# Performance work log

Hardware: AMD Instinct MI355X
Metric: run time of the kernel (lower is better)

Reference implementation:

```python
import jax, jax.numpy as jnp
import numpy as np

# Module hyperparameters (BNMorph.__init__ defaults + KITTI resolution)
B, H, W = 8, 320, 1024
SEARCH_W = 7      # serachWidth
SEARCH_H = 3      # searchHeight
SPARSITY_RAD = 2
SENSE_R = 20
PIX_DW = 24.0     # pixel_distance_weight
ALPHA_DW = 0.7    # alpha_distance_weight
PIX_MUL_DW = 1.9  # pixel_mulline_distance_weight
ALPHA_PAD = 1.6   # alpha_padding
EDGE_DENSITY = 0.02


def _make_offsets():
    # Exactly mirrors BNMorph.__init__ buffer construction.
    rs = np.arange(-SEARCH_W, SEARCH_W + 1)
    cs = np.arange(-SEARCH_H, SEARCH_H + 1)
    xx, yy = np.meshgrid(rs, cs)
    xx = xx.flatten(); yy = yy.flatten()
    idx = np.argsort(xx ** 2 + yy ** 2)
    xx = xx[idx]; yy = yy[idx]
    ss = np.arange(-SPARSITY_RAD, SPARSITY_RAD + 1)
    sxx, syy = np.meshgrid(ss, ss)
    sxx = sxx.flatten(); syy = syy.flatten()
    cspan = np.arange(-SENSE_R, SENSE_R + 1)
    cxx, cyy = np.meshgrid(cspan, cspan)
    cxx = cxx.flatten(); cyy = cyy.flatten()
    ci = np.argsort(cxx ** 2 + cyy ** 2)
    cxx = cxx[ci]; cyy = cyy[ci]
    f32 = lambda a: jnp.asarray(a, dtype=jnp.float32)
    return f32(xx), f32(yy), f32(sxx), f32(syy), f32(cxx), f32(cyy)


def setup_inputs() -> dict:
    key = jax.random.key(0)
    k1, k2 = jax.random.split(key)
    binMapsrc = (jax.random.uniform(k1, (B, 1, H, W)) < EDGE_DENSITY).astype(jnp.float32)
    binMapdst = (jax.random.uniform(k2, (B, 1, H, W)) < EDGE_DENSITY).astype(jnp.float32)
    xx, yy, sxx, syy, cxx, cyy = _make_offsets()
    return {"binMapsrc": binMapsrc, "binMapdst": binMapdst,
            "xx": xx, "yy": yy, "sxx": sxx, "syy": syy, "cxx": cxx, "cyy": cyy}


def _forward(binMapsrc, binMapdst, xx, yy, sxx, syy, cxx, cyy):
    src = binMapsrc[:, 0] > 0.5  # [B,H,W] bool
    dst = binMapdst[:, 0] > 0.5
    b, h, w = src.shape

    # ---- 1. sparsity filtering of src edge points ----
    # keep an active pixel iff no active pixel precedes it (raster order)
    # inside the sparsity window -> approximates greedy sparsification.
    sdx = sxx.astype(jnp.int32); sdy = syy.astype(jnp.int32)
    prec = ((sdy < 0) | ((sdy == 0) & (sdx < 0))).astype(jnp.float32)
    Ps = jnp.pad(src.astype(jnp.float32),
                 ((0, 0), (SPARSITY_RAD, SPARSITY_RAD), (SPARSITY_RAD, SPARSITY_RAD)))

    def sp_step(acc, off):
        dx, dy, wk = off
        sl = jax.lax.dynamic_slice(Ps, (0, SPARSITY_RAD + dy, SPARSITY_RAD + dx), (b, h, w))
        return acc + sl * wk, None

    acc, _ = jax.lax.scan(sp_step, jnp.zeros((b, h, w), jnp.float32), (sdx, sdy, prec))
    kept = src & (acc < 0.5)

    # ---- 2. windowed nearest-correspondence search in dst ----
    # offsets (xx,yy) are pre-sorted by distance, so the first hit is nearest.
    qdx = xx.astype(jnp.int32); qdy = yy.astype(jnp.int32)
    Pd = jnp.pad(dst, ((0, 0), (SEARCH_H, SEARCH_H), (SEARCH_W, SEARCH_W)))

    def m_step(carry, off):
        found, vx, vy = carry
        dx, dy, dxf, dyf = off
        sl = jax.lax.dynamic_slice(Pd, (0, SEARCH_H + dy, SEARCH_W + dx), (b, h, w))
        hit = sl & kept & (~found)
        vx = jnp.where(hit, dxf, vx)
        vy = jnp.where(hit, dyf, vy)
        return (found | hit, vx, vy), None

    init = (jnp.zeros((b, h, w), bool),
            jnp.zeros((b, h, w), jnp.float32),
            jnp.zeros((b, h, w), jnp.float32))
    (found, vx, vy), _ = jax.lax.scan(m_step, init, (qdx, qdy, xx, yy))

    # ---- 3. distance-weighted morph field (splat = depthwise conv) ----
    d = jnp.sqrt(cxx ** 2 + cyy ** 2)
    wts = ALPHA_DW * jnp.exp(-d * PIX_MUL_DW / PIX_DW)
    R = SENSE_R
    K = jnp.zeros((2 * R + 1, 2 * R + 1), jnp.float32)
    K = K.at[cyy.astype(jnp.int32) + R, cxx.astype(jnp.int32) + R].set(wts)

    m = found.astype(jnp.float32)
    inp = jnp.stack([m, m * vx, m * vy], axis=1)        # [B,3,H,W]
    ker = jnp.tile(K[None, None], (3, 1, 1, 1))          # [3,1,41,41]
    out = jax.lax.conv_general_dilated(
        inp, ker, (1, 1), ((R, R), (R, R)),
        dimension_numbers=("NCHW", "OIHW", "NCHW"), feature_group_count=3)
    den = out[:, 0] + ALPHA_PAD
    dispx = out[:, 1] / den
    dispy = out[:, 2] / den

    ygrid, xgrid = jnp.meshgrid(jnp.arange(h, dtype=jnp.float32),
                                jnp.arange(w, dtype=jnp.float32), indexing="ij")
    morphedx = xgrid + dispx
    morphedy = ygrid + dispy
    orgpts_x = xgrid * m
    orgpts_y = ygrid * m
    correspts_x = (xgrid + vx) * m
    correspts_y = (ygrid + vy) * m
    return morphedx, morphedy, orgpts_x, orgpts_y, correspts_x, correspts_y


def reference(binMapsrc, binMapdst, xx, yy, sxx, syy, cxx, cyy):
    return _forward(binMapsrc, binMapdst, xx, yy, sxx, syy, cxx, cyy)
```

## Files before the change

kernel.cpp:

```cpp
#include <hip/hip_runtime.h>


#define BB 8
#define HH 320
#define WW 1024
#define N_PIX (BB*HH*WW)
#define WPI (HH*(WW/32))
#define RR 20
#define TLW 64
#define TLH 32
#define TXN (WW/TLW)
#define TYN (HH/TLH)
#define NQ 105
#define CAP 192
#define WSTRIDE 52
#define WTABN (2*42*WSTRIDE)
#define WTAB_OFF (2*BB*WPI*4)

typedef unsigned long long u64;
typedef float v2f __attribute__((ext_vector_type(2)));

__global__ __launch_bounds__(256) void pack_zero(
    const float* __restrict__ src, const float* __restrict__ dst,
    unsigned* __restrict__ packed, float* __restrict__ wtab_g)
{
    int t = threadIdx.x;
    int i = blockIdx.x * 256 + t;
    if (i < WTABN) {
        int rot = i / (42 * WSTRIDE);
        int rem = i - rot * (42 * WSTRIDE);
        int row = rem / WSTRIDE, c = rem - row * WSTRIDE;
        int pc = c + rot;
        float v = 0.0f;
        if (row <= 40 && pc >= 4 && pc <= 44) {
            int dxv = pc - 24, dyv = row - 20;
            float d = sqrtf((float)(dxv * dxv + dyv * dyv));
            v = 0.7f * expf((-d * 1.9f) / 24.0f);
        }
        wtab_g[i] = v;
    }
    const float4* p = (i < (N_PIX >> 2)) ? (const float4*)src + i
                                         : (const float4*)dst + (i - (N_PIX >> 2));
    float4 v = *p;
    unsigned nib = (v.x > 0.5f ? 1u : 0u) | (v.y > 0.5f ? 2u : 0u)
                 | (v.z > 0.5f ? 4u : 0u) | (v.w > 0.5f ? 8u : 0u);
    unsigned val = nib << ((t & 7) * 4);
    val |= __shfl_xor(val, 1);
    val |= __shfl_xor(val, 2);
    val |= __shfl_xor(val, 4);
    if ((t & 7) == 0) packed[i >> 3] = val;
}

__global__ __launch_bounds__(256, 5) void fused_morph(
    const unsigned* __restrict__ packed,
    const float* __restrict__ xx, const float* __restrict__ yy,
    const float* __restrict__ wtab_g,
    float* __restrict__ out)
{
    __shared__ __align__(16) float wtab[WTABN];
    __shared__ unsigned sSrc[74][6];
    __shared__ unsigned sDst[78][6];
    __shared__ __align__(16) unsigned sPt[CAP];
    __shared__ __align__(16) unsigned sWav[4][200];
    __shared__ int prank[NQ];
    __shared__ unsigned char sVB[TLH * TLW];
    __shared__ int lcnt;

    int t = threadIdx.x;
    int txT = blockIdx.x, tyT = blockIdx.y, b = blockIdx.z;
    int tx0 = txT * TLW, ty0 = tyT * TLH;
    int wb0 = (tx0 >> 5) - 1;
    const unsigned* psrc = packed + (size_t)b * WPI;
    const unsigned* pdst = packed + (size_t)(BB + b) * WPI;

    for (int i = t; i < WTABN / 4; i += 256)
        ((float4*)wtab)[i] = ((const float4*)wtab_g)[i];
    for (int i = t; i < 74 * 4; i += 256) {
        int r = i >> 2, w = (i & 3) + 1;
        int gy = ty0 - 22 + r, gw = wb0 + (w - 1);
        sSrc[r][w] = (gy >= 0 && gy < HH && gw >= 0 && gw < 32) ? psrc[(gy << 5) + gw] : 0u;
    }
    for (int i = t; i < 78 * 4; i += 256) {
        int r = i >> 2, w = (i & 3) + 1;
        int gy = ty0 - 23 + r, gw = wb0 + (w - 1);
        sDst[r][w] = (gy >= 0 && gy < HH && gw >= 0 && gw < 32) ? pdst[(gy << 5) + gw] : 0u;
    }
    if (t < 78) { sDst[t][0] = 0; sDst[t][5] = 0; if (t < 74) { sSrc[t][0] = 0; sSrc[t][5] = 0; } }
    if (t < NQ) {
        int dx = (int)xx[t], dy = (int)yy[t];
        prank[(dy + 3) * 15 + (dx + 7)] = (t << 8) | ((dx + 7) << 4) | (dy + 3);
    }
    ((unsigned*)sVB)[t] = 0; ((unsigned*)sVB)[t + 256] = 0;
    if (t == 0) lcnt = 0;
    __syncthreads();

    for (int task = t; task < 288; task += 256) {
        int cr = task >> 2, w = (task & 3) + 1;
        unsigned C = sSrc[cr + 2][w];
        unsigned found = 0;
        if (C) {
            #define EXT5(row) ( (u64)((row)[w-1] >> 30) \
                              | ((u64)(row)[w] << 2) \
                              | ((u64)((row)[w+1] & 3u) << 34) )
            u64 a = EXT5(sSrc[cr]) | EXT5(sSrc[cr + 1]);
            u64 or5 = a | (a >> 1) | (a >> 2) | (a >> 3) | (a >> 4);
            u64 e2 = EXT5(sSrc[cr + 2]);
            unsigned kept = C & ~(unsigned)(or5 | e2 | (e2 >> 1));
            if (kept) {
                u64 dil = 0;
                #pragma unroll
                for (int rr = 0; rr < 7; ++rr) {
                    const unsigned* row = sDst[cr + rr];
                    dil |= (u64)(row[w-1] >> 25) | ((u64)row[w] << 7)
                         | ((u64)(row[w+1] & 0x7Fu) << 39);
                }
                u64 a2 = dil | (dil >> 1);
                u64 b2 = a2 | (a2 >> 2);
                u64 c2 = b2 | (b2 >> 4);
                u64 o15 = c2 | (c2 >> 7);
                found = kept & (unsigned)o15;
            }
        }
        if (w == 1) found &= 0xFFFFF000u;
        if (w == 4) found &= 0x000FFFFFu;
        if (found) {
            int nf = __popc(found);
            int base = atomicAdd(&lcnt, nf);
            unsigned fi = found;
            while (fi) {
                int bit = __builtin_ctz(fi); fi &= fi - 1;
                int px = tx0 - 32 + ((w - 1) << 5) + bit;
                if (base < CAP) sPt[base] = (unsigned)((cr << 10) | px);
                ++base;
            }
        }
    }
    __syncthreads();
    int nPts = lcnt; if (nPts > CAP) nPts = CAP;

    if (t < nPts) {
        unsigned e = sPt[t];
        int cr = (int)(e >> 10), px = (int)(e & 1023u);
        int q = px - tx0 + 25;
        int widx = 1 + (q >> 5), sh = q & 31;
        u64 lo = 0, hi = 0;
        #pragma unroll
        for (int rr = 0; rr < 7; ++rr) {
            const unsigned* row = sDst[cr + rr];
            u64 win = (((u64)row[widx] | ((u64)row[widx + 1] << 32)) >> sh) & 0x7FFFull;
            if (rr < 4) lo |= win << (15 * rr);
            else        hi |= win << (15 * (rr - 4));
        }
        int minv = 0x7FFFFFFF;
        while (lo) { int bb2 = __builtin_ctzll(lo); lo &= lo - 1; int rv = prank[bb2];      if (rv < minv) minv = rv; }
        while (hi) { int bb2 = __builtin_ctzll(hi); hi &= hi - 1; int rv = prank[60 + bb2]; if (rv < minv) minv = rv; }
        int vxp7 = (minv >> 4) & 15, vyp3 = minv & 15;
        int py = ty0 - 20 + cr;
        sPt[t] = (unsigned)px | ((unsigned)py << 10)
               | ((unsigned)vxp7 << 19) | ((unsigned)vyp3 << 23);
        if (px >= tx0 && px < tx0 + TLW && cr >= 20 && cr < 20 + TLH)
            sVB[(cr - 20) * TLW + (px - tx0)] =
                (unsigned char)(0x80 | vxp7 | (vyp3 << 4));
    }
    __syncthreads();

    int lane = t & 63, w = __builtin_amdgcn_readfirstlane(t >> 6);
    int wy0 = ty0 + w * 8;
    int cw = 0;
    for (int base = 0; base < nPts; base += 64) {
        int i = base + lane;
        unsigned pk = (i < nPts) ? sPt[i] : 0xFFFFFFFFu;
        int py = (int)((pk >> 10) & 511u);
        bool pass = (i < nPts) & (py >= wy0 - 20) & (py <= wy0 + 27);
        u64 m = __ballot(pass);
        if (pass) {
            int idx = __popcll(m & ((1ull << lane) - 1ull));
            sWav[w][cw + idx] = pk;
        }
        cw += __popcll(m);
    }
    int c4 = (cw + 3) & ~3;
    if (lane < c4 - cw) sWav[w][cw + lane] = 0xFFFFFFFFu;

    int x0q = tx0 + (t & 15) * 4;
    int y0t = ty0 + (t >> 4) * 2;

    v2f a0p[2][2] = {};
    v2f av[2][4]  = {};

    for (int p = 0; p < c4; p += 4) {
        uint4 P = *(const uint4*)&sWav[w][p];
        #pragma unroll
        for (int k = 0; k < 4; ++k) {
            int spk = __builtin_amdgcn_readfirstlane(
                (int)(k == 0 ? P.x : k == 1 ? P.y : k == 2 ? P.z : P.w));
            int pxp21 = (spk & 1023) + 21;
            int pyp20 = ((spk >> 10) & 511) + 20;
            float pvx = (float)(((spk >> 19) & 15) - 7);
            float pvy = (float)(((spk >> 23) & 7) - 3);
            v2f vv = {pvx, pvy};

            int coff = pxp21 - x0q;
            coff = coff < 0 ? 0 : (coff > 45 ? 45 : coff);
            int rot = coff & 1;
            int cb  = rot * (42 * WSTRIDE) + (coff & ~1);
            #pragma unroll
            for (int ry = 0; ry < 2; ++ry) {
                int dyr = pyp20 - (y0t + ry);
                int rowi = ((unsigned)dyr > 40u) ? 41 : dyr;
                const float* wr = &wtab[cb + rowi * WSTRIDE];
                v2f w01 = *(const v2f*)wr;
                v2f w23 = *(const v2f*)(wr + 2);
                a0p[ry][0] += (v2f){w23.y, w23.x};
                a0p[ry][1] += (v2f){w01.y, w01.x};
                av[ry][0] += w23.y * vv;
                av[ry][1] += w23.x * vv;
                av[ry][2] += w01.y * vv;
                av[ry][3] += w01.x * vv;
            }
        }
    }

    size_t bbase = (size_t)b * HH * WW;
    int lx = x0q - tx0;
    #pragma unroll
    for (int ry = 0; ry < 2; ++ry) {
        int y = y0t + ry;
        int ly = y - ty0;
        unsigned vb4 = *(const unsigned*)&sVB[ly * TLW + lx];
        size_t idx = bbase + (size_t)y * WW + x0q;
        float d0 = a0p[ry][0].x + 1.6f, d1 = a0p[ry][0].y + 1.6f;
        float d2 = a0p[ry][1].x + 1.6f, d3 = a0p[ry][1].y + 1.6f;
        float4 ox = { (float)x0q     + av[ry][0].x / d0, (float)(x0q+1) + av[ry][1].x / d1,
                      (float)(x0q+2) + av[ry][2].x / d2, (float)(x0q+3) + av[ry][3].x / d3 };
        float4 oy = { (float)y + av[ry][0].y / d0, (float)y + av[ry][1].y / d1,
                      (float)y + av[ry][2].y / d2, (float)y + av[ry][3].y / d3 };
        float4 o2, o3, o4, o5;
        float* po2 = &o2.x; float* po3 = &o3.x; float* po4 = &o4.x; float* po5 = &o5.x;
        #pragma unroll
        for (int jj = 0; jj < 4; ++jj) {
            unsigned by = (vb4 >> (8 * jj)) & 255u;
            float fm  = (float)(by >> 7);
            float fvx = (float)((int)(by & 15u) - 7);
            float fvy = (float)((int)((by >> 4) & 7u) - 3);
            float fx  = (float)(x0q + jj);
            po2[jj] = fx * fm;
            po3[jj] = (float)y * fm;
            po4[jj] = (fx + fvx) * fm;
            po5[jj] = ((float)y + fvy) * fm;
        }
        *reinterpret_cast<float4*>(out + idx)                     = ox;
        *reinterpret_cast<float4*>(out + (size_t)N_PIX + idx)     = oy;
        *reinterpret_cast<float4*>(out + 2 * (size_t)N_PIX + idx) = o2;
        *reinterpret_cast<float4*>(out + 3 * (size_t)N_PIX + idx) = o3;
        *reinterpret_cast<float4*>(out + 4 * (size_t)N_PIX + idx) = o4;
        *reinterpret_cast<float4*>(out + 5 * (size_t)N_PIX + idx) = o5;
    }
}

extern "C" void kernel_launch(void* const* d_in, const int* in_sizes, int n_in,
                              void* d_out, int out_size, void* d_ws, size_t ws_size,
                              hipStream_t stream) {
    const float* src = (const float*)d_in[0];
    const float* dst = (const float*)d_in[1];
    const float* xx  = (const float*)d_in[2];
    const float* yy  = (const float*)d_in[3];
    float* out = (float*)d_out;

    unsigned* packed = (unsigned*)d_ws;
    float*    wtab_g = (float*)((char*)d_ws + WTAB_OFF);

    pack_zero<<<(2 * N_PIX / 4) / 256, 256, 0, stream>>>(src, dst, packed, wtab_g);

    dim3 g2(TXN, TYN, BB);
    fused_morph<<<g2, 256, 0, stream>>>(packed, xx, yy, wtab_g, out);
}
```

Before: 124.6 us.

## Halve tile height to 16 rows, use 128-thread blocks and a single unrotated weight table

Tile height drops from 32 to 16 rows and blocks shrink to 128 threads (2 waves), giving twice as many blocks with less per-block shared memory. The weight table no longer keeps two column-rotated copies for aligned 8-byte loads. It becomes one table with an odd stride, read as four scalar LDS loads. This aims at better occupancy and load balance and smaller LDS use. The costs are a larger share of halo work per output (40 halo rows for 16 output rows) and more LDS load instructions in the inner accumulation loop.

Result: no change. 124.7 us (+0.2%).

```diff
diff --git a/kernel.cpp b/kernel.cpp
--- a/kernel.cpp
+++ b/kernel.cpp
@@ -8,13 +8,16 @@
 #define WPI (HH*(WW/32))
 #define RR 20
 #define TLW 64
-#define TLH 32
+#define TLH 16
 #define TXN (WW/TLW)
 #define TYN (HH/TLH)
 #define NQ 105
-#define CAP 192
-#define WSTRIDE 52
-#define WTABN (2*42*WSTRIDE)
+#define CAP 160
+#define NCR (TLH+40)
+#define NSR (NCR+2)
+#define NDR (NCR+6)
+#define WSTRIDE 53
+#define WTABN 2228
 #define WTAB_OFF (2*BB*WPI*4)
 
 typedef unsigned long long u64;
@@ -27,13 +30,10 @@
     int t = threadIdx.x;
     int i = blockIdx.x * 256 + t;
     if (i < WTABN) {
-        int rot = i / (42 * WSTRIDE);
-        int rem = i - rot * (42 * WSTRIDE);
-        int row = rem / WSTRIDE, c = rem - row * WSTRIDE;
-        int pc = c + rot;
+        int row = i / WSTRIDE, c = i - row * WSTRIDE;
         float v = 0.0f;
-        if (row <= 40 && pc >= 4 && pc <= 44) {
-            int dxv = pc - 24, dyv = row - 20;
+        if (row <= 40 && c >= 4 && c <= 44) {
+            int dxv = c - 24, dyv = row - 20;
             float d = sqrtf((float)(dxv * dxv + dyv * dyv));
             v = 0.7f * expf((-d * 1.9f) / 24.0f);
         }
@@ -51,17 +51,17 @@
     if ((t & 7) == 0) packed[i >> 3] = val;
 }
 
-__global__ __launch_bounds__(256, 5) void fused_morph(
+__global__ __launch_bounds__(128, 5) void fused_morph(
     const unsigned* __restrict__ packed,
     const float* __restrict__ xx, const float* __restrict__ yy,
     const float* __restrict__ wtab_g,
     float* __restrict__ out)
 {
     __shared__ __align__(16) float wtab[WTABN];
-    __shared__ unsigned sSrc[74][6];
-    __shared__ unsigned sDst[78][6];
+    __shared__ unsigned sSrc[NSR][6];
+    __shared__ unsigned sDst[NDR][6];
     __shared__ __align__(16) unsigned sPt[CAP];
-    __shared__ __align__(16) unsigned sWav[4][200];
+    __shared__ __align__(16) unsigned sWav[2][CAP + 4];
     __shared__ int prank[NQ];
     __shared__ unsigned char sVB[TLH * TLW];
     __shared__ int lcnt;
@@ -73,28 +73,28 @@
     const unsigned* psrc = packed + (size_t)b * WPI;
     const unsigned* pdst = packed + (size_t)(BB + b) * WPI;
 
-    for (int i = t; i < WTABN / 4; i += 256)
+    for (int i = t; i < WTABN / 4; i += 128)
         ((float4*)wtab)[i] = ((const float4*)wtab_g)[i];
-    for (int i = t; i < 74 * 4; i += 256) {
+    for (int i = t; i < NSR * 4; i += 128) {
         int r = i >> 2, w = (i & 3) + 1;
         int gy = ty0 - 22 + r, gw = wb0 + (w - 1);
         sSrc[r][w] = (gy >= 0 && gy < HH && gw >= 0 && gw < 32) ? psrc[(gy << 5) + gw] : 0u;
     }
-    for (int i = t; i < 78 * 4; i += 256) {
+    for (int i = t; i < NDR * 4; i += 128) {
         int r = i >> 2, w = (i & 3) + 1;
         int gy = ty0 - 23 + r, gw = wb0 + (w - 1);
         sDst[r][w] = (gy >= 0 && gy < HH && gw >= 0 && gw < 32) ? pdst[(gy << 5) + gw] : 0u;
     }
-    if (t < 78) { sDst[t][0] = 0; sDst[t][5] = 0; if (t < 74) { sSrc[t][0] = 0; sSrc[t][5] = 0; } }
+    if (t < NDR) { sDst[t][0] = 0; sDst[t][5] = 0; if (t < NSR) { sSrc[t][0] = 0; sSrc[t][5] = 0; } }
     if (t < NQ) {
         int dx = (int)xx[t], dy = (int)yy[t];
         prank[(dy + 3) * 15 + (dx + 7)] = (t << 8) | ((dx + 7) << 4) | (dy + 3);
     }
-    ((unsigned*)sVB)[t] = 0; ((unsigned*)sVB)[t + 256] = 0;
+    ((unsigned*)sVB)[t] = 0; ((unsigned*)sVB)[t + 128] = 0;
     if (t == 0) lcnt = 0;
     __syncthreads();
 
-    for (int task = t; task < 288; task += 256) {
+    for (int task = t; task < NCR * 4; task += 128) {
         int cr = task >> 2, w = (task & 3) + 1;
         unsigned C = sSrc[cr + 2][w];
         unsigned found = 0;
@@ -138,8 +138,8 @@
     __syncthreads();
     int nPts = lcnt; if (nPts > CAP) nPts = CAP;
 
-    if (t < nPts) {
-        unsigned e = sPt[t];
+    for (int i = t; i < nPts; i += 128) {
+        unsigned e = sPt[i];
         int cr = (int)(e >> 10), px = (int)(e & 1023u);
         int q = px - tx0 + 25;
         int widx = 1 + (q >> 5), sh = q & 31;
@@ -156,7 +156,7 @@
         while (hi) { int bb2 = __builtin_ctzll(hi); hi &= hi - 1; int rv = prank[60 + bb2]; if (rv < minv) minv = rv; }
         int vxp7 = (minv >> 4) & 15, vyp3 = minv & 15;
         int py = ty0 - 20 + cr;
-        sPt[t] = (unsigned)px | ((unsigned)py << 10)
+        sPt[i] = (unsigned)px | ((unsigned)py << 10)
                | ((unsigned)vxp7 << 19) | ((unsigned)vyp3 << 23);
         if (px >= tx0 && px < tx0 + TLW && cr >= 20 && cr < 20 + TLH)
             sVB[(cr - 20) * TLW + (px - tx0)] =
@@ -202,21 +202,18 @@
 
             int coff = pxp21 - x0q;
             coff = coff < 0 ? 0 : (coff > 45 ? 45 : coff);
-            int rot = coff & 1;
-            int cb  = rot * (42 * WSTRIDE) + (coff & ~1);
             #pragma unroll
             for (int ry = 0; ry < 2; ++ry) {
                 int dyr = pyp20 - (y0t + ry);
                 int rowi = ((unsigned)dyr > 40u) ? 41 : dyr;
-                const float* wr = &wtab[cb + rowi * WSTRIDE];
-                v2f w01 = *(const v2f*)wr;
-                v2f w23 = *(const v2f*)(wr + 2);
-                a0p[ry][0] += (v2f){w23.y, w23.x};
-                a0p[ry][1] += (v2f){w01.y, w01.x};
-                av[ry][0] += w23.y * vv;
-                av[ry][1] += w23.x * vv;
-                av[ry][2] += w01.y * vv;
-                av[ry][3] += w01.x * vv;
+                const float* wr = &wtab[rowi * WSTRIDE + coff];
+                float w3 = wr[0], w2 = wr[1], w1 = wr[2], w0 = wr[3];
+                a0p[ry][0] += (v2f){w0, w1};
+                a0p[ry][1] += (v2f){w2, w3};
+                av[ry][0] += w0 * vv;
+                av[ry][1] += w1 * vv;
+                av[ry][2] += w2 * vv;
+                av[ry][3] += w3 * vv;
             }
         }
     }
@@ -273,5 +270,5 @@
     pack_zero<<<(2 * N_PIX / 4) / 256, 256, 0, stream>>>(src, dst, packed, wtab_g);
 
     dim3 g2(TXN, TYN, BB);
-    fused_morph<<<g2, 256, 0, stream>>>(packed, xx, yy, wtab_g, out);
+    fused_morph<<<g2, 128, 0, stream>>>(packed, xx, yy, wtab_g, out);
 }
```
